# Kernel optimization log

Measured on AMD Instinct MI355X. Metric: run time of the kernel, lower is better.

Reference implementation:

```python
import jax, jax.numpy as jnp
import numpy as np

NEG = jnp.float32(-1e7)

def _rel_attend(node, W, adj):
    # node: [B,N,H], W: [H,H], adj: [B,N,N] int
    scores = jnp.einsum('bnh,hk,bmk->bnm', node, W, node)
    scores = jnp.where(adj == 1, scores, NEG)
    att = jax.nn.softmax(scores, axis=2)
    return jnp.einsum('bnm,bmh->bnh', att, node)

def setup_inputs() -> dict:
    key = jax.random.key(0)
    ks = jax.random.split(key, 8)
    B, N, H = 8, 1024, 768
    return {
        'node_embedding': jax.random.normal(ks[0], (B, N, H), dtype=jnp.float32),
        'adjacent_matrix_refer': jax.random.randint(ks[1], (B, N, N), 0, 2, dtype=jnp.int32),
        'adjacent_matrix_occur': jax.random.randint(ks[2], (B, N, N), 0, 2, dtype=jnp.int32),
        'adjacent_matrix_update': jax.random.randint(ks[3], (B, N, N), 0, 2, dtype=jnp.int32),
        'params_refer': jax.random.normal(ks[4], (H, H), dtype=jnp.float32),
        'params_occur': jax.random.normal(ks[5], (H, H), dtype=jnp.float32),
        'params_update': jax.random.normal(ks[6], (H, H), dtype=jnp.float32),
        'params': jax.random.normal(ks[7], (3 * H, H), dtype=jnp.float32),
    }

def reference(node_embedding, adjacent_matrix_refer, adjacent_matrix_occur,
              adjacent_matrix_update, params_refer, params_occur,
              params_update, params):
    w_refer = _rel_attend(node_embedding, params_refer, adjacent_matrix_refer)
    w_occur = _rel_attend(node_embedding, params_occur, adjacent_matrix_occur)
    w_update = _rel_attend(node_embedding, params_update, adjacent_matrix_update)
    w_cat = jnp.concatenate((w_refer, w_occur, w_update), axis=2)  # [B,N,3H]
    return jnp.einsum('bnk,kh->bnh', w_cat, params)
```

## Files before the change

kernel.cpp:

```cpp
#include <hip/hip_runtime.h>
#include <stdint.h>

typedef _Float16 f16_t;
typedef _Float16 f16x8 __attribute__((ext_vector_type(8)));
typedef _Float16 f16x4 __attribute__((ext_vector_type(4)));
typedef float f32x4 __attribute__((ext_vector_type(4)));

#define GLL16(g, l)                                                                   \
  __builtin_amdgcn_global_load_lds((const __attribute__((address_space(1))) uint32_t*)(g), \
                                   (__attribute__((address_space(3))) uint32_t*)(l),  \
                                   16, 0, 0)

#define NP_PANEL 98304L
#define NP_KT    4096L
#define WP_Z     589824L
#define TP_SLOT  6291456L
#define TP_PANEL 196608L
#define TP_KT    8192L

#define EPI_COORDS                              \
  const int tid  = threadIdx.x;                 \
  const int wave = tid >> 6;                    \
  const int lane = tid & 63;                    \
  const int lm   = lane & 15;                   \
  const int q    = lane >> 4;                   \
  const int wi   = (wave >> 1) * 64;            \
  const int wj   = (wave & 1) * 64;

#define ZERO_ACC(acc)                                            \
  _Pragma("unroll") for (int i = 0; i < 4; ++i)                  \
  _Pragma("unroll") for (int j = 0; j < 4; ++j)                  \
    acc[i][j] = (f32x4){0.f, 0.f, 0.f, 0.f};

__device__ __forceinline__ void gemm_tile_pb(const f16_t* __restrict__ A, long lda,
                                             const f16_t* __restrict__ Bp,
                                             int kTiles, f16_t* lA, f16_t* lB,
                                             f32x4 acc[4][4])
{
  const int tid  = threadIdx.x;
  const int wave = tid >> 6;
  const int lane = tid & 63;

  const f16_t* pA[4];
  const f16_t* pB[4];
  f16_t* lAb[4];
  f16_t* lBb[4];
#pragma unroll
  for (int i = 0; i < 4; ++i) {
    int c  = i * 256 + tid;
    int m  = c & 127;
    int kq = c >> 7;
    pA[i]  = A + (long)m * lda + kq * 8;
    pB[i]  = Bp + (long)c * 8;
    int cb = i * 256 + wave * 64;
    lAb[i] = lA + (long)cb * 8;
    lBb[i] = lB + (long)cb * 8;
  }
  const int lm = lane & 15;
  const int q  = lane >> 4;
  const int wi = (wave >> 1) * 64;
  const int wj = (wave & 1) * 64;

  for (int kt = 0; kt < kTiles; ++kt) {
    long koA = (long)kt * 64;
    long koB = (long)kt * 8192;
#pragma unroll
    for (int i = 0; i < 4; ++i) GLL16(pA[i] + koA, lAb[i]);
#pragma unroll
    for (int i = 0; i < 4; ++i) GLL16(pB[i] + koB, lBb[i]);
    __syncthreads();
#pragma unroll
    for (int s = 0; s < 2; ++s) {
      f16x8 af[4], bfr[4];
#pragma unroll
      for (int i = 0; i < 4; ++i)
        af[i] = *(const f16x8*)(lA + (((s * 4 + q) * 128) + wi + i * 16 + lm) * 8);
#pragma unroll
      for (int j = 0; j < 4; ++j)
        bfr[j] = *(const f16x8*)(lB + (((s * 4 + q) * 128) + wj + j * 16 + lm) * 8);
#pragma unroll
      for (int i = 0; i < 4; ++i)
#pragma unroll
        for (int j = 0; j < 4; ++j)
          acc[i][j] = __builtin_amdgcn_mfma_f32_16x16x32_f16(af[i], bfr[j], acc[i][j], 0, 0, 0);
    }
    __syncthreads();
  }
}

__device__ __forceinline__ void gemm_tile3_p(const f16_t* __restrict__ Ahp,
                                             const f16_t* __restrict__ Alp,
                                             const f16_t* __restrict__ Bhp,
                                             const f16_t* __restrict__ Blp,
                                             int kTiles,
                                             f16_t* lAh, f16_t* lAl,
                                             f16_t* lBh, f16_t* lBl,
                                             f32x4 acc[4][4])
{
  const int tid  = threadIdx.x;
  const int wave = tid >> 6;
  const int lane = tid & 63;

  const f16_t* pAh[2]; const f16_t* pAl[2];
  const f16_t* pBh[2]; const f16_t* pBl[2];
  f16_t* dAh[2]; f16_t* dAl[2]; f16_t* dBh[2]; f16_t* dBl[2];
#pragma unroll
  for (int i = 0; i < 2; ++i) {
    int c  = i * 256 + tid;
    pAh[i] = Ahp + (long)c * 8;  pAl[i] = Alp + (long)c * 8;
    pBh[i] = Bhp + (long)c * 8;  pBl[i] = Blp + (long)c * 8;
    int cb = i * 256 + wave * 64;
    dAh[i] = lAh + (long)cb * 8;  dAl[i] = lAl + (long)cb * 8;
    dBh[i] = lBh + (long)cb * 8;  dBl[i] = lBl + (long)cb * 8;
  }
  const int lm = lane & 15;
  const int q  = lane >> 4;
  const int wi = (wave >> 1) * 64;
  const int wj = (wave & 1) * 64;

  for (int kt = 0; kt < kTiles; ++kt) {
    long ko = (long)kt * NP_KT;
#pragma unroll
    for (int i = 0; i < 2; ++i) GLL16(pAh[i] + ko, dAh[i]);
#pragma unroll
    for (int i = 0; i < 2; ++i) GLL16(pAl[i] + ko, dAl[i]);
#pragma unroll
    for (int i = 0; i < 2; ++i) GLL16(pBh[i] + ko, dBh[i]);
#pragma unroll
    for (int i = 0; i < 2; ++i) GLL16(pBl[i] + ko, dBl[i]);
    __syncthreads();
    {
      f16x8 ah[4], al[4], bh[4], bl[4];
#pragma unroll
      for (int i = 0; i < 4; ++i)
        ah[i] = *(const f16x8*)(lAh + (q * 128 + wi + i * 16 + lm) * 8);
#pragma unroll
      for (int j = 0; j < 4; ++j)
        bh[j] = *(const f16x8*)(lBh + (q * 128 + wj + j * 16 + lm) * 8);
#pragma unroll
      for (int i = 0; i < 4; ++i)
#pragma unroll
        for (int j = 0; j < 4; ++j)
          acc[i][j] = __builtin_amdgcn_mfma_f32_16x16x32_f16(ah[i], bh[j], acc[i][j], 0, 0, 0);
#pragma unroll
      for (int i = 0; i < 4; ++i)
        al[i] = *(const f16x8*)(lAl + (q * 128 + wi + i * 16 + lm) * 8);
#pragma unroll
      for (int i = 0; i < 4; ++i)
#pragma unroll
        for (int j = 0; j < 4; ++j)
          acc[i][j] = __builtin_amdgcn_mfma_f32_16x16x32_f16(al[i], bh[j], acc[i][j], 0, 0, 0);
#pragma unroll
      for (int j = 0; j < 4; ++j)
        bl[j] = *(const f16x8*)(lBl + (q * 128 + wj + j * 16 + lm) * 8);
#pragma unroll
      for (int i = 0; i < 4; ++i)
#pragma unroll
        for (int j = 0; j < 4; ++j)
          acc[i][j] = __builtin_amdgcn_mfma_f32_16x16x32_f16(ah[i], bl[j], acc[i][j], 0, 0, 0);
    }
    __syncthreads();
  }
}


#define SC8_MFMA_QUAD(i0, j0)                                                   \
  __builtin_amdgcn_s_setprio(1);                                                \
  _Pragma("unroll") for (int ii = 0; ii < 2; ++ii)                              \
  _Pragma("unroll") for (int jj = 0; jj < 2; ++jj) {                            \
    acc[(i0)+ii][(j0)+jj] = __builtin_amdgcn_mfma_f32_16x16x32_f16(             \
        ah[(i0)+ii], bh[(j0)+jj], acc[(i0)+ii][(j0)+jj], 0, 0, 0);              \
    acc[(i0)+ii][(j0)+jj] = __builtin_amdgcn_mfma_f32_16x16x32_f16(             \
        al[(i0)+ii], bh[(j0)+jj], acc[(i0)+ii][(j0)+jj], 0, 0, 0);              \
    acc[(i0)+ii][(j0)+jj] = __builtin_amdgcn_mfma_f32_16x16x32_f16(             \
        ah[(i0)+ii], bl[(j0)+jj], acc[(i0)+ii][(j0)+jj], 0, 0, 0);              \
  }                                                                             \
  __builtin_amdgcn_s_setprio(0);

#define SC8_RD_A(lb, i)                                                \
  ah[i] = *(const f16x8*)((lb) + raA + (i) * 128);                     \
  al[i] = *(const f16x8*)((lb) + 8192 + raA + (i) * 128);
#define SC8_RD_B(lb, j)                                                \
  bh[j] = *(const f16x8*)((lb) + 16384 + rbB + (j) * 128);             \
  bl[j] = *(const f16x8*)((lb) + 20480 + rbB + (j) * 128);

#define SC8_BAR_LGKM                                                   \
  __builtin_amdgcn_s_barrier();                                        \
  asm volatile("s_waitcnt lgkmcnt(0)" ::: "memory");

#define SC8_STAGE_TILE(nb, T)                                    \
  {                                                              \
    long koA = (long)(T) * TP_KT;                                \
    long koB = (long)(T) * NP_KT;                                \
    GLL16(pAh0 + koA, (nb) + dA0);                               \
    GLL16(pAh1 + koA, (nb) + dA1);                               \
    GLL16(pAl0 + koA, (nb) + 8192 + dA0);                        \
    GLL16(pAl1 + koA, (nb) + 8192 + dA1);                        \
    GLL16(pBh + koB, (nb) + 16384 + dB);                         \
    GLL16(pBl + koB, (nb) + 20480 + dB);                         \
  }

#define SC8_TILE(LB, NB, T, ST)                                                 \
  {                                                                             \
    const f16_t* lb = (LB);                                                     \
    f16_t* nb = (NB);                                                           \
    const long koA = (long)((T) + 2) * TP_KT;                                   \
    const long koB = (long)((T) + 2) * NP_KT;                                   \
    f16x8 ah[4], al[4], bh[4], bl[4];                                           \
    SC8_RD_A(lb, 0); SC8_RD_A(lb, 1); SC8_RD_B(lb, 0); SC8_RD_B(lb, 1);         \
    if (ST) { GLL16(pAh0 + koA, nb + dA0); GLL16(pAh1 + koA, nb + dA1); }       \
    SC8_BAR_LGKM;                                                               \
    SC8_MFMA_QUAD(0, 0);                                                        \
    __builtin_amdgcn_s_barrier();                                               \
    SC8_RD_B(lb, 2); SC8_RD_B(lb, 3);                                           \
    if (ST) { GLL16(pAl0 + koA, nb + 8192 + dA0); GLL16(pAl1 + koA, nb + 8192 + dA1); } \
    SC8_BAR_LGKM;                                                               \
    SC8_MFMA_QUAD(0, 2);                                                        \
    __builtin_amdgcn_s_barrier();                                               \
    SC8_RD_A(lb, 2); SC8_RD_A(lb, 3);                                           \
    if (ST) GLL16(pBh + koB, nb + 16384 + dB);                                  \
    SC8_BAR_LGKM;                                                               \
    SC8_MFMA_QUAD(2, 2);                                                        \
    __builtin_amdgcn_s_barrier();                                               \
    if (ST) GLL16(pBl + koB, nb + 20480 + dB);                                  \
    SC8_BAR_LGKM;                                                               \
    SC8_MFMA_QUAD(2, 0);                                                        \
  }

#define SC8_WAIT6_BAR                                                  \
  asm volatile("s_waitcnt vmcnt(6)" ::: "memory");                     \
  __builtin_amdgcn_s_barrier();
#define SC8_WAIT0_BAR                                                  \
  asm volatile("s_waitcnt vmcnt(0)" ::: "memory");                     \
  __builtin_amdgcn_s_barrier();

__device__ __forceinline__ void mainloop8_3p(const f16_t* __restrict__ Ahp,
                                             const f16_t* __restrict__ Alp,
                                             const f16_t* __restrict__ Bhp,
                                             const f16_t* __restrict__ Blp,
                                             f16_t* lds, f32x4 acc[4][4])
{
  f16_t* bu0 = lds;
  f16_t* bu1 = lds + 24576;
  f16_t* bu2 = lds + 49152;

  const int tid  = threadIdx.x;
  const int wave = tid >> 6;
  const int lane = tid & 63;
  const int lm   = lane & 15;
  const int q    = lane >> 4;
  const int wm   = wave >> 1;
  const int wn   = wave & 1;

  const f16_t* pAh0 = Ahp + (long)tid * 8;
  const f16_t* pAh1 = Ahp + (long)(tid + 512) * 8;
  const f16_t* pAl0 = Alp + (long)tid * 8;
  const f16_t* pAl1 = Alp + (long)(tid + 512) * 8;
  const f16_t* pBh = Bhp + (long)tid * 8;
  const f16_t* pBl = Blp + (long)tid * 8;
  const int dA0 = wave * 512;
  const int dA1 = 4096 + wave * 512;
  const int dB  = wave * 512;

  const int raA = (q * 256 + wm * 64 + lm) * 8;
  const int rbB = (q * 128 + wn * 64 + lm) * 8;

  SC8_STAGE_TILE(bu0, 0);
  SC8_STAGE_TILE(bu1, 1);
  SC8_WAIT6_BAR;

  for (int it = 0; it < 7; ++it) {
    int t0 = it * 3;
    SC8_TILE(bu0, bu2, t0, 1);     SC8_WAIT6_BAR;
    SC8_TILE(bu1, bu0, t0 + 1, 1); SC8_WAIT6_BAR;
    SC8_TILE(bu2, bu1, t0 + 2, 1); SC8_WAIT6_BAR;
  }
  SC8_TILE(bu0, bu2, 21, 1); SC8_WAIT6_BAR;
  SC8_TILE(bu1, bu0, 22, 0); SC8_WAIT0_BAR;
  SC8_TILE(bu2, bu1, 23, 0);
}

__global__ __launch_bounds__(256) void k_cvt_split(const float* __restrict__ src,
                                                   f16_t* __restrict__ hi,
                                                   f16_t* __restrict__ lo)
{
  const int kt    = blockIdx.x;
  const int panel = blockIdx.y;
  const int t     = threadIdx.x;
  long pbase = ((long)panel * 24 + kt) * NP_KT;
#pragma unroll
  for (int i = 0; i < 2; ++i) {
    int c  = i * 256 + t;
    int m  = c & 127;
    int kq = c >> 7;
    const float* sp = src + ((long)panel * 128 + m) * 768 + kt * 32 + kq * 8;
    float4 u = *(const float4*)sp;
    float4 w = *(const float4*)(sp + 4);
    f16_t h0 = (f16_t)u.x, h1 = (f16_t)u.y, h2 = (f16_t)u.z, h3 = (f16_t)u.w;
    f16_t h4 = (f16_t)w.x, h5 = (f16_t)w.y, h6 = (f16_t)w.z, h7 = (f16_t)w.w;
    f16x8 hv = {h0, h1, h2, h3, h4, h5, h6, h7};
    f16x8 lv = {(f16_t)(u.x - (float)h0), (f16_t)(u.y - (float)h1),
                (f16_t)(u.z - (float)h2), (f16_t)(u.w - (float)h3),
                (f16_t)(w.x - (float)h4), (f16_t)(w.y - (float)h5),
                (f16_t)(w.z - (float)h6), (f16_t)(w.w - (float)h7)};
    *(f16x8*)(hi + pbase + (long)c * 8) = hv;
    *(f16x8*)(lo + pbase + (long)c * 8) = lv;
  }
}

__global__ __launch_bounds__(256) void k_transpose_all(const float* __restrict__ w0,
                                                       const float* __restrict__ w1,
                                                       const float* __restrict__ w2,
                                                       const float* __restrict__ params,
                                                       f16_t* __restrict__ Wh,
                                                       f16_t* __restrict__ Wl,
                                                       f16_t* __restrict__ paramsT)
{
  __shared__ float t[32][33];
  const int z = blockIdx.z;
  const float* src;
  int C;
  if (z < 3) {
    if (blockIdx.y >= 24) return;
    src = (z == 0) ? w0 : ((z == 1) ? w1 : w2);
    C = 768;
  } else {
    src = params;
    C = 768;
  }
  int x = blockIdx.x * 32 + threadIdx.x;
  int y = blockIdx.y * 32 + threadIdx.y;
#pragma unroll
  for (int j = 0; j < 32; j += 8)
    t[threadIdx.y + j][threadIdx.x] = src[(long)(y + j) * C + x];
  __syncthreads();
  int x2 = blockIdx.y * 32 + threadIdx.x;
  int y2 = blockIdx.x * 32 + threadIdx.y;
  if (z < 3) {
    f16_t* hi = Wh + (long)z * WP_Z;
    f16_t* lo = Wl + (long)z * WP_Z;
#pragma unroll
    for (int j = 0; j < 32; j += 8) {
      float v  = t[threadIdx.x][threadIdx.y + j];
      int row = y2 + j;
      int col = x2;
      f16_t h  = (f16_t)v;
      long off = (long)(row >> 7) * NP_PANEL + (long)(col >> 5) * NP_KT +
                 (long)((col >> 3) & 3) * 1024 + (long)(row & 127) * 8 + (col & 7);
      hi[off] = h;
      lo[off] = (f16_t)(v - (float)h);
    }
  } else {
#pragma unroll
    for (int j = 0; j < 32; j += 8) {
      float v  = t[threadIdx.x][threadIdx.y + j];
      long idx = (long)(y2 + j) * 2304 + x2;
      paramsT[idx] = (f16_t)v;
    }
  }
}

__global__ __launch_bounds__(256, 4) void k_tw_vt(const f16_t* __restrict__ nh,
                                                  const f16_t* __restrict__ nl,
                                                  const f16_t* __restrict__ Wh,
                                                  const f16_t* __restrict__ Wl,
                                                  const f16_t* __restrict__ paramsT,
                                                  f16_t* __restrict__ Thi,
                                                  f16_t* __restrict__ Tlo,
                                                  f16_t* __restrict__ Vt,
                                                  int br_base, int g)
{
  __shared__ __align__(16) f16_t lds[16384];
  if ((int)blockIdx.z < g) {
    f32x4 acc[4][4];
    ZERO_ACC(acc);
    const int slot = blockIdx.z;
    const long br  = br_base + slot;
    const f16_t* Ahp = nh + (long)blockIdx.x * NP_PANEL;
    const f16_t* Alp = nl + (long)blockIdx.x * NP_PANEL;
    const f16_t* Bhp = Wh + br * WP_Z + (long)blockIdx.y * NP_PANEL;
    const f16_t* Blp = Wl + br * WP_Z + (long)blockIdx.y * NP_PANEL;
    gemm_tile3_p(Ahp, Alp, Bhp, Blp, 24,
                 lds, lds + 4096, lds + 8192, lds + 12288, acc);
    EPI_COORDS;
    long out0 = (long)slot * TP_SLOT;
    long row0 = (long)blockIdx.x * 128;
    long col0 = (long)blockIdx.y * 128;
#pragma unroll
    for (int i = 0; i < 4; ++i)
#pragma unroll
      for (int j = 0; j < 4; ++j)
#pragma unroll
        for (int r = 0; r < 4; ++r) {
          long row = row0 + wi + i * 16 + q * 4 + r;
          long col = col0 + wj + j * 16 + lm;
          float v  = acc[i][j][r];
          f16_t h  = (f16_t)v;
          long off = out0 + (row >> 8) * TP_PANEL + (col >> 5) * TP_KT +
                     ((col >> 3) & 3) * 2048 + (row & 255) * 8 + (col & 7);
          Thi[off] = h;
          Tlo[off] = (f16_t)(v - (float)h);
        }
  } else {
    int id   = blockIdx.x + 64 * (blockIdx.y + 6 * (blockIdx.z - g));
    int vx   = id % 6;
    int rest = id / 6;
    int vy   = rest & 7;
    int vz   = rest >> 3;
    int b    = vz & 7;
    int br   = vz >> 3;
    f32x4 acc[4][4];
    ZERO_ACC(acc);
    const f16_t* A  = paramsT + (long)vx * 128 * 2304 + (long)br * 768;
    const f16_t* Bp = nh + (long)(b * 8 + vy) * NP_PANEL;
    gemm_tile_pb(A, 2304, Bp, 12, lds, lds + 8192, acc);
    EPI_COORDS;
    f16_t* C = Vt + ((long)(br * 8 + b) * 768) * 1024;
    long row0 = (long)vx * 128;
    long col0 = (long)vy * 128;
#pragma unroll
    for (int i = 0; i < 4; ++i)
#pragma unroll
      for (int j = 0; j < 4; ++j)
#pragma unroll
        for (int r = 0; r < 4; ++r) {
          long row = row0 + wi + i * 16 + q * 4 + r;
          long col = col0 + wj + j * 16 + lm;
          C[row * 1024 + col] = (f16_t)acc[i][j][r];
        }
  }
}

__global__ __launch_bounds__(512, 2) void k_gemm_scores8(const f16_t* __restrict__ Thi,
                                                         const f16_t* __restrict__ Tlo,
                                                         const f16_t* __restrict__ nh,
                                                         const f16_t* __restrict__ nl,
                                                         const int* __restrict__ adj0,
                                                         const int* __restrict__ adj1,
                                                         const int* __restrict__ adj2,
                                                         float* __restrict__ S, int br_base)
{
  __shared__ __align__(16) f16_t lds[3 * 24576];

  const int tid  = threadIdx.x;
  const int wave = tid >> 6;
  const int lane = tid & 63;
  const int lm   = lane & 15;
  const int q    = lane >> 4;
  const int wm   = wave >> 1;
  const int wn   = wave & 1;

  const int nblk  = 32 * (int)gridDim.y;
  const int chunk = nblk >> 3;
  int lid = (int)blockIdx.x + 32 * (int)blockIdx.y;
  int swz = (lid & 7) * chunk + (lid >> 3);
  const int zz = swz >> 5;
  const int mt = (swz >> 3) & 3;
  const int nt = swz & 7;
  const int b    = zz & 7;
  const int slot = zz >> 3;

  const f16_t* Ahp = Thi + (long)slot * TP_SLOT + (long)(b * 4 + mt) * TP_PANEL;
  const f16_t* Alp = Tlo + (long)slot * TP_SLOT + (long)(b * 4 + mt) * TP_PANEL;
  const f16_t* Bhp = nh + (long)(b * 8 + nt) * NP_PANEL;
  const f16_t* Blp = nl + (long)(b * 8 + nt) * NP_PANEL;

  f32x4 acc[4][4];
  ZERO_ACC(acc);
  mainloop8_3p(Ahp, Alp, Bhp, Blp, lds, acc);

  const int br   = br_base + slot;
  const int* adj = (br == 0) ? adj0 : ((br == 1) ? adj1 : adj2);
  const int* adjb = adj + (long)b * 1024 * 1024;
  float* Sb = S + ((long)slot * 8 + b) * 1024 * 1024;
  long row0 = (long)mt * 256 + wm * 64;
  long col0 = (long)nt * 128 + wn * 64;
#pragma unroll
  for (int i = 0; i < 4; ++i)
#pragma unroll
    for (int j = 0; j < 4; ++j)
#pragma unroll
      for (int r = 0; r < 4; ++r) {
        long row = row0 + i * 16 + q * 4 + r;
        long col = col0 + j * 16 + lm;
        float v  = acc[i][j][r];
        v = (adjb[row * 1024 + col] == 1) ? v : -1e7f;
        Sb[row * 1024 + col] = v;
      }
}

__global__ __launch_bounds__(256) void k_softmax(float* __restrict__ S)
{
  const int wave = threadIdx.x >> 6;
  const int lane = threadIdx.x & 63;
  long row = (long)blockIdx.x * 4 + wave;
  float* rowp = S + row * 1024;
  float4 v[4];
#pragma unroll
  for (int i = 0; i < 4; ++i) v[i] = ((const float4*)rowp)[lane + 64 * i];
  float m = -3e38f;
#pragma unroll
  for (int i = 0; i < 4; ++i)
    m = fmaxf(m, fmaxf(fmaxf(v[i].x, v[i].y), fmaxf(v[i].z, v[i].w)));
#pragma unroll
  for (int off = 32; off; off >>= 1) m = fmaxf(m, __shfl_xor(m, off));
  float e[4][4];
  float s = 0.f;
#pragma unroll
  for (int i = 0; i < 4; ++i) {
    e[i][0] = __expf(v[i].x - m);
    e[i][1] = __expf(v[i].y - m);
    e[i][2] = __expf(v[i].z - m);
    e[i][3] = __expf(v[i].w - m);
    s += e[i][0] + e[i][1] + e[i][2] + e[i][3];
  }
#pragma unroll
  for (int off = 32; off; off >>= 1) s += __shfl_xor(s, off);
  float inv = 1.0f / s;
  f16_t* orow = (f16_t*)rowp;
#pragma unroll
  for (int i = 0; i < 4; ++i) {
    f16x4 o = {(f16_t)(e[i][0] * inv), (f16_t)(e[i][1] * inv),
               (f16_t)(e[i][2] * inv), (f16_t)(e[i][3] * inv)};
    *(f16x4*)(orow + (lane + 64 * i) * 4) = o;
  }
}

__global__ __launch_bounds__(256, 2) void k_gemm_pvf(const float* __restrict__ S,
                                                     const f16_t* __restrict__ Vt,
                                                     float* __restrict__ out,
                                                     int g, int br_base)
{
  __shared__ __align__(16) f16_t lds[3 * 12288];
  const int tid  = threadIdx.x;
  const int wave = tid >> 6;
  const int lane = tid & 63;
  const int lm   = lane & 15;
  const int q    = lane >> 4;
  const int wi   = (wave >> 1) * 64;
  const int wj   = (wave & 1) * 32;
  const int b    = blockIdx.z;
  const int TT   = 16 * g;

  long aoff[4];
  int  adst[4];
#pragma unroll
  for (int i = 0; i < 4; ++i) {
    int c   = i * 256 + tid;
    int m   = c & 127;
    int kq  = c >> 7;
    aoff[i] = (long)m * 2048 + kq * 8;
    adst[i] = (i * 256 + wave * 64) * 8;
  }
  long boff[2];
  int  bdst[2];
#pragma unroll
  for (int i = 0; i < 2; ++i) {
    int c   = i * 256 + tid;
    int m   = c & 63;
    int kq  = c >> 6;
    boff[i] = (long)m * 1024 + kq * 8;
    bdst[i] = 8192 + (i * 256 + wave * 64) * 8;
  }
  const long abase = ((long)b * 1024 + (long)blockIdx.x * 128) * 2048;
  const long bcol  = (long)blockIdx.y * 64 * 1024;

  f32x4 acc[4][2];
#pragma unroll
  for (int i = 0; i < 4; ++i)
#pragma unroll
    for (int j = 0; j < 2; ++j)
      acc[i][j] = (f32x4){0.f, 0.f, 0.f, 0.f};

#define PVF_STAGE(TG, BUF)                                                     \
  {                                                                            \
    int slot_ = (TG) >> 4;                                                     \
    long ko_  = (long)((TG) & 15) * 64;                                        \
    const f16_t* As_ = (const f16_t*)(S + (long)slot_ * 8 * 1024 * 1024) + abase; \
    const f16_t* Bs_ = Vt + (((long)(br_base + slot_) * 8 + b) * 768) * 1024 + bcol; \
    f16_t* L_ = lds + (BUF) * 12288;                                           \
    GLL16(As_ + aoff[0] + ko_, L_ + adst[0]);                                  \
    GLL16(As_ + aoff[1] + ko_, L_ + adst[1]);                                  \
    GLL16(As_ + aoff[2] + ko_, L_ + adst[2]);                                  \
    GLL16(As_ + aoff[3] + ko_, L_ + adst[3]);                                  \
    GLL16(Bs_ + boff[0] + ko_, L_ + bdst[0]);                                  \
    GLL16(Bs_ + boff[1] + ko_, L_ + bdst[1]);                                  \
  }

#define PVF_COMPUTE(BUF)                                                       \
  {                                                                            \
    const f16_t* L_ = lds + (BUF) * 12288;                                     \
    _Pragma("unroll") for (int s2 = 0; s2 < 2; ++s2) {                         \
      f16x8 af[4], bfr[2];                                                     \
      _Pragma("unroll") for (int i = 0; i < 4; ++i)                            \
        af[i] = *(const f16x8*)(L_ + (((s2 * 4 + q) * 128) + wi + i * 16 + lm) * 8); \
      _Pragma("unroll") for (int j = 0; j < 2; ++j)                            \
        bfr[j] = *(const f16x8*)(L_ + 8192 + (((s2 * 4 + q) * 64) + wj + j * 16 + lm) * 8); \
      _Pragma("unroll") for (int i = 0; i < 4; ++i)                            \
        _Pragma("unroll") for (int j = 0; j < 2; ++j)                          \
          acc[i][j] = __builtin_amdgcn_mfma_f32_16x16x32_f16(af[i], bfr[j], acc[i][j], 0, 0, 0); \
    }                                                                          \
  }

  PVF_STAGE(0, 0);
  PVF_STAGE(1, 1);
  asm volatile("s_waitcnt vmcnt(6)" ::: "memory");
  __builtin_amdgcn_s_barrier();

  int buf = 0;
  for (int tg = 0; tg < TT; ++tg) {
    int nb = buf + 2; if (nb >= 3) nb -= 3;
    if (tg + 2 < TT) PVF_STAGE(tg + 2, nb);
    PVF_COMPUTE(buf);
    if (tg + 2 < TT) {
      asm volatile("s_waitcnt vmcnt(6)" ::: "memory");
    } else if (tg + 1 < TT) {
      asm volatile("s_waitcnt vmcnt(0)" ::: "memory");
    }
    __builtin_amdgcn_s_barrier();
    ++buf; if (buf == 3) buf = 0;
  }
#undef PVF_STAGE
#undef PVF_COMPUTE

  float* Cb = out + (long)b * 1024 * 768;
  long row0 = (long)blockIdx.x * 128;
  long col0 = (long)blockIdx.y * 64;
#pragma unroll
  for (int i = 0; i < 4; ++i)
#pragma unroll
    for (int j = 0; j < 2; ++j)
#pragma unroll
      for (int r = 0; r < 4; ++r) {
        long row = row0 + wi + i * 16 + q * 4 + r;
        long col = col0 + wj + j * 16 + lm;
        float v  = acc[i][j][r];
        if (br_base != 0) v += Cb[row * 768 + col];
        Cb[row * 768 + col] = v;
      }
}

extern "C" void kernel_launch(void* const* d_in, const int* in_sizes, int n_in,
                              void* d_out, int out_size, void* d_ws, size_t ws_size,
                              hipStream_t stream)
{
  const float* node    = (const float*)d_in[0];
  const int*   adjp[3] = {(const int*)d_in[1], (const int*)d_in[2], (const int*)d_in[3]};
  const float* Wp[3]   = {(const float*)d_in[4], (const float*)d_in[5], (const float*)d_in[6]};
  const float* params  = (const float*)d_in[7];
  float* out = (float*)d_out;

  const size_t SZ_W3 = 3ull * 768 * 768 * 2;
  const size_t SZ_PT = 768ull * 2304 * 2;
  const size_t SZ_N  = 8192ull * 768 * 2;
  const size_t SZ_VT = 24ull * 768 * 1024 * 2;
  const size_t SZ_T  = 8192ull * 768 * 2;
  const size_t SZ_S  = 8ull * 1024 * 1024 * 4;
  const size_t FIXED = 2 * SZ_W3 + SZ_PT + 2 * SZ_N + SZ_VT;
  const size_t SLOT  = 2 * SZ_T + SZ_S;

  int NBR = 1;
  if (ws_size >= FIXED + 3 * SLOT) NBR = 3;
  else if (ws_size >= FIXED + 2 * SLOT) NBR = 2;
  else if (ws_size < FIXED + SLOT) return;

  char* base = (char*)d_ws;
  size_t off = 0;
  f16_t* Wh      = (f16_t*)(base + off); off += SZ_W3;
  f16_t* Wl      = (f16_t*)(base + off); off += SZ_W3;
  f16_t* paramsT = (f16_t*)(base + off); off += SZ_PT;
  f16_t* node_hi = (f16_t*)(base + off); off += SZ_N;
  f16_t* node_lo = (f16_t*)(base + off); off += SZ_N;
  f16_t* Vt      = (f16_t*)(base + off); off += SZ_VT;
  f16_t* Thi     = (f16_t*)(base + off); off += (size_t)NBR * SZ_T;
  f16_t* Tlo     = (f16_t*)(base + off); off += (size_t)NBR * SZ_T;
  float* S       = (float*)(base + off); off += (size_t)NBR * SZ_S;

  k_cvt_split<<<dim3(24, 64, 1), 256, 0, stream>>>(node, node_hi, node_lo);
  k_transpose_all<<<dim3(24, 72, 4), dim3(32, 8), 0, stream>>>(Wp[0], Wp[1], Wp[2], params,
                                                               Wh, Wl, paramsT);

  int done = 0;
  while (done < 3) {
    int g = (3 - done < NBR) ? (3 - done) : NBR;
    int vtz = (done == 0) ? 3 : 0;
    k_tw_vt<<<dim3(64, 6, g + vtz), 256, 0, stream>>>(node_hi, node_lo, Wh, Wl, paramsT,
                                                      Thi, Tlo, Vt, done, g);
    k_gemm_scores8<<<dim3(32, 8 * g, 1), 512, 0, stream>>>(Thi, Tlo, node_hi, node_lo,
                                                           adjp[0], adjp[1], adjp[2], S, done);
    k_softmax<<<2048 * g, 256, 0, stream>>>(S);
    k_gemm_pvf<<<dim3(8, 12, 8), 256, 0, stream>>>(S, Vt, out, g, done);
    done += g;
  }
}
```

Baseline: 523.1 us.

## Pre-panelize paramsT and use row-contiguous XOR-swizzled loads in PV GEMM

The transpose kernel now writes paramsT in a packed panel layout, so the V-projection GEMM can stream contiguous 8 KB k-tiles for A as it already does for B. The PV kernel's global-to-LDS loads now read 8 consecutive 16-byte chunks per row instead of strided column chunks, with an XOR swizzle on the chunk index so the LDS fragment reads stay free of bank conflicts. The aim is better global coalescing and fewer LDS bank conflicts. It adds index arithmetic, and correctness depends on the swizzle used for the LDS stores matching the one used for the reads.

```diff
diff --git a/kernel.cpp b/kernel.cpp
--- a/kernel.cpp
+++ b/kernel.cpp
@@ -17,6 +17,7 @@
 #define TP_SLOT  6291456L
 #define TP_PANEL 196608L
 #define TP_KT    8192L
+#define PT_VXBR  98304L
 
 #define EPI_COORDS                              \
   const int tid  = threadIdx.x;                 \
@@ -32,7 +33,7 @@
   _Pragma("unroll") for (int j = 0; j < 4; ++j)                  \
     acc[i][j] = (f32x4){0.f, 0.f, 0.f, 0.f};
 
-__device__ __forceinline__ void gemm_tile_pb(const f16_t* __restrict__ A, long lda,
+__device__ __forceinline__ void gemm_tile_pp(const f16_t* __restrict__ Ap,
                                              const f16_t* __restrict__ Bp,
                                              int kTiles, f16_t* lA, f16_t* lB,
                                              f32x4 acc[4][4])
@@ -48,9 +49,7 @@
 #pragma unroll
   for (int i = 0; i < 4; ++i) {
     int c  = i * 256 + tid;
-    int m  = c & 127;
-    int kq = c >> 7;
-    pA[i]  = A + (long)m * lda + kq * 8;
+    pA[i]  = Ap + (long)c * 8;
     pB[i]  = Bp + (long)c * 8;
     int cb = i * 256 + wave * 64;
     lAb[i] = lA + (long)cb * 8;
@@ -62,12 +61,11 @@
   const int wj = (wave & 1) * 64;
 
   for (int kt = 0; kt < kTiles; ++kt) {
-    long koA = (long)kt * 64;
-    long koB = (long)kt * 8192;
-#pragma unroll
-    for (int i = 0; i < 4; ++i) GLL16(pA[i] + koA, lAb[i]);
-#pragma unroll
-    for (int i = 0; i < 4; ++i) GLL16(pB[i] + koB, lBb[i]);
+    long ko = (long)kt * 8192;
+#pragma unroll
+    for (int i = 0; i < 4; ++i) GLL16(pA[i] + ko, lAb[i]);
+#pragma unroll
+    for (int i = 0; i < 4; ++i) GLL16(pB[i] + ko, lBb[i]);
     __syncthreads();
 #pragma unroll
     for (int s = 0; s < 2; ++s) {
@@ -354,8 +352,15 @@
 #pragma unroll
     for (int j = 0; j < 32; j += 8) {
       float v  = t[threadIdx.x][threadIdx.y + j];
-      long idx = (long)(y2 + j) * 2304 + x2;
-      paramsT[idx] = (f16_t)v;
+      int r  = y2 + j;
+      int c  = x2;
+      int vx = r >> 7, m = r & 127;
+      int br = c / 768;
+      int cc = c - br * 768;
+      int kt = cc >> 6, kq = (cc >> 3) & 7, e = cc & 7;
+      long off = (long)(vx * 3 + br) * PT_VXBR + (long)kt * 8192 +
+                 (long)(kq * 128 + m) * 8 + e;
+      paramsT[off] = (f16_t)v;
     }
   }
 }
@@ -411,9 +416,9 @@
     int br   = vz >> 3;
     f32x4 acc[4][4];
     ZERO_ACC(acc);
-    const f16_t* A  = paramsT + (long)vx * 128 * 2304 + (long)br * 768;
+    const f16_t* Ap = paramsT + (long)(vx * 3 + br) * PT_VXBR;
     const f16_t* Bp = nh + (long)(b * 8 + vy) * NP_PANEL;
-    gemm_tile_pb(A, 2304, Bp, 12, lds, lds + 8192, acc);
+    gemm_tile_pp(Ap, Bp, 12, lds, lds + 8192, acc);
     EPI_COORDS;
     f16_t* C = Vt + ((long)(br * 8 + b) * 768) * 1024;
     long row0 = (long)vx * 128;
@@ -547,9 +552,9 @@
 #pragma unroll
   for (int i = 0; i < 4; ++i) {
     int c   = i * 256 + tid;
-    int m   = c & 127;
-    int kq  = c >> 7;
-    aoff[i] = (long)m * 2048 + kq * 8;
+    int rw  = c >> 3;
+    int cg  = (c & 7) ^ (rw & 7);
+    aoff[i] = (long)rw * 2048 + cg * 8;
     adst[i] = (i * 256 + wave * 64) * 8;
   }
   long boff[2];
@@ -557,9 +562,9 @@
 #pragma unroll
   for (int i = 0; i < 2; ++i) {
     int c   = i * 256 + tid;
-    int m   = c & 63;
-    int kq  = c >> 6;
-    boff[i] = (long)m * 1024 + kq * 8;
+    int rw  = c >> 3;
+    int cg  = (c & 7) ^ (rw & 7);
+    boff[i] = (long)rw * 1024 + cg * 8;
     bdst[i] = 8192 + (i * 256 + wave * 64) * 8;
   }
   const long abase = ((long)b * 1024 + (long)blockIdx.x * 128) * 2048;
@@ -591,11 +596,12 @@
   {                                                                            \
     const f16_t* L_ = lds + (BUF) * 12288;                                     \
     _Pragma("unroll") for (int s2 = 0; s2 < 2; ++s2) {                         \
+      const int kx = (s2 * 4 + q) ^ (lm & 7);                                  \
       f16x8 af[4], bfr[2];                                                     \
       _Pragma("unroll") for (int i = 0; i < 4; ++i)                            \
-        af[i] = *(const f16x8*)(L_ + (((s2 * 4 + q) * 128) + wi + i * 16 + lm) * 8); \
+        af[i] = *(const f16x8*)(L_ + (wi + i * 16 + lm) * 64 + kx * 8);        \
       _Pragma("unroll") for (int j = 0; j < 2; ++j)                            \
-        bfr[j] = *(const f16x8*)(L_ + 8192 + (((s2 * 4 + q) * 64) + wj + j * 16 + lm) * 8); \
+        bfr[j] = *(const f16x8*)(L_ + 8192 + (wj + j * 16 + lm) * 64 + kx * 8); \
       _Pragma("unroll") for (int i = 0; i < 4; ++i)                            \
         _Pragma("unroll") for (int j = 0; j < 2; ++j)                          \
           acc[i][j] = __builtin_amdgcn_mfma_f32_16x16x32_f16(af[i], bfr[j], acc[i][j], 0, 0, 0); \
```

Result: faster. 472.8 us (-9.6%).
